# Kernel optimization log

Measured on AMD Instinct MI355X. Metric: run time of the kernel, lower is better.

## Reference

```python
import jax, jax.numpy as jnp
import numpy as np

EMBED = 2048
N_EXPERTS = 64
TOP_K = 8


def setup_inputs() -> dict:
    key = jax.random.key(0)
    k_x, k_w, k_b = jax.random.split(key, 3)
    inputs = jax.random.normal(k_x, (8, 4096, EMBED), dtype=jnp.float32)
    # nn.Linear(embed_size, num_experts): weight [E, D], bias [E]
    bound = 1.0 / np.sqrt(EMBED)
    W = jax.random.uniform(k_w, (N_EXPERTS, EMBED), dtype=jnp.float32, minval=-bound, maxval=bound)
    b = jax.random.uniform(k_b, (N_EXPERTS,), dtype=jnp.float32, minval=-bound, maxval=bound)
    return {"inputs": inputs, "W": W, "b": b}


def reference(inputs, W, b):
    # scores: [B, S, E]
    scores = jnp.einsum("bsd,ed->bse", inputs, W) + b
    topk_scores, indices = jax.lax.top_k(scores, TOP_K)  # [B,S,K]
    # scatter topk_scores into a zero mask (non-selected slots stay 0.0)
    onehot = jax.nn.one_hot(indices, N_EXPERTS, dtype=scores.dtype)  # [B,S,K,E]
    mask = jnp.einsum("bske,bsk->bse", onehot, topk_scores)
    router_output = jax.nn.softmax(mask, axis=-1)
    return (router_output, indices)
```

## Files before the change

kernel.cpp:

```cpp
#include <hip/hip_runtime.h>
#include <math.h>

#define N_TOKENS 32768
#define EMBED    2048
#define NEXP     64
#define TOPK     8
#define BM       64
#define BK       64
#define NCH      (EMBED / BK)
#define SCS      65
#define THRESH   1e-4f
#define WELEMS   (NEXP * EMBED)

typedef __attribute__((ext_vector_type(8)))  short short8;
typedef __attribute__((ext_vector_type(4)))  short short4v;
typedef __attribute__((ext_vector_type(16))) float f32x16;

__device__ __forceinline__ unsigned short bf16rne(float f) {
  unsigned int fb = __float_as_uint(f);
  return (unsigned short)((fb + 0x7FFFu + ((fb >> 16) & 1u)) >> 16);
}

__device__ __forceinline__ void cvt4(float4 f, short4v* h, short4v* l) {
  float fs[4] = {f.x, f.y, f.z, f.w};
  short4v hh, ll;
#pragma unroll
  for (int i = 0; i < 4; ++i) {
    unsigned short hr = bf16rne(fs[i]);
    hh[i] = (short)hr;
    float hf = __uint_as_float((unsigned int)hr << 16);
    ll[i] = (short)bf16rne(fs[i] - hf);
  }
  *h = hh; *l = ll;
}

__global__ void split_w(const float* __restrict__ W, short* __restrict__ wh,
                        short* __restrict__ wl) {
  const int T = blockIdx.x * 256 + threadIdx.x;
  const int n = T >> 8, kg8 = T & 255;
  const float4* W4 = (const float4*)W;
  float4 a = W4[n * 512 + kg8 * 2];
  float4 b = W4[n * 512 + kg8 * 2 + 1];
  short4v h0, l0, h1, l1;
  cvt4(a, &h0, &l0); cvt4(b, &h1, &l1);
  short* dh = &wh[(kg8 * 64 + n) * 8];
  short* dl = &wl[(kg8 * 64 + n) * 8];
  *(short4v*)dh = h0; *(short4v*)(dh + 4) = h1;
  *(short4v*)dl = l0; *(short4v*)(dl + 4) = l1;
}

__global__ __launch_bounds__(256, 4)
void router_kernel(const float* __restrict__ x, const short* __restrict__ wh,
                   const short* __restrict__ wl, const float* __restrict__ bias,
                   const float* __restrict__ Wf, float* __restrict__ out) {
  __shared__ float4 lx[2][1024];
  __shared__ double s_fix[NEXP];
  __shared__ int    s_list[BM];
  __shared__ int    s_cnt;
  float* sc = (float*)&lx[0][0];

  const int tid  = threadIdx.x;
  const int t0   = blockIdx.x * BM;
  const int lane = tid & 63;
  const int w    = tid >> 6;
  const int half = lane >> 5;
  const int r5   = lane & 31;
  const int tw   = (w & 1) * 32;
  const int ew   = (w >> 1) * 32;

  if (tid == 0) s_cnt = 0;

  const float4* x4g = (const float4*)x;
  const short8* Bh  = (const short8*)wh;
  const short8* Bl  = (const short8*)wl;
  const int boff = half * 64 + ew + r5;

  const int row16 = tid >> 4;
  const int s4    = tid & 15;
  const int c4sw  = s4 ^ row16;
  const int wbase = (tid & 192);

  f32x16 acc;
#pragma unroll
  for (int i = 0; i < 16; ++i) acc[i] = 0.f;

#pragma unroll
  for (int i = 0; i < 4; ++i) {
    const float4* gp = x4g + (size_t)(t0 + row16 + 16 * i) * (EMBED / 4) + c4sw;
    __builtin_amdgcn_global_load_lds((const void*)gp, (void*)&lx[0][i * 256 + wbase],
                                     16, 0, 0);
  }

  const int arow  = tw + r5;
  const int am    = arow & 15;
  const int abase = (arow >> 4) * 256 + am * 16;

  for (int ch = 0; ch < NCH; ++ch) {
    const int buf = ch & 1;
    __syncthreads();

    if (ch + 1 < NCH) {
#pragma unroll
      for (int i = 0; i < 4; ++i) {
        const float4* gp = x4g + (size_t)(t0 + row16 + 16 * i) * (EMBED / 4)
                               + (ch + 1) * 16 + c4sw;
        __builtin_amdgcn_global_load_lds((const void*)gp,
                                         (void*)&lx[buf ^ 1][i * 256 + wbase], 16, 0, 0);
      }
    }

    short8 bh[4], bl[4];
#pragma unroll
    for (int s = 0; s < 4; ++s) {
      const int bi = (ch * 4 + s) * 128 + boff;
      bh[s] = Bh[bi]; bl[s] = Bl[bi];
    }

#pragma unroll
    for (int s = 0; s < 4; ++s) {
      const int c0 = s * 4 + half * 2;
      float4 fa = lx[buf][abase + (c0 ^ am)];
      float4 fb = lx[buf][abase + ((c0 + 1) ^ am)];
      short4v h0, l0, h1, l1;
      cvt4(fa, &h0, &l0); cvt4(fb, &h1, &l1);
      short8 ah, al;
#pragma unroll
      for (int j = 0; j < 4; ++j) { ah[j] = h0[j]; ah[j + 4] = h1[j];
                                    al[j] = l0[j]; al[j + 4] = l1[j]; }
      acc = __builtin_amdgcn_mfma_f32_32x32x16_bf16(ah, bh[s], acc, 0, 0, 0);
      acc = __builtin_amdgcn_mfma_f32_32x32x16_bf16(ah, bl[s], acc, 0, 0, 0);
      acc = __builtin_amdgcn_mfma_f32_32x32x16_bf16(al, bh[s], acc, 0, 0, 0);
    }
  }

  __syncthreads();

#pragma unroll
  for (int reg = 0; reg < 16; ++reg) {
    const int row = (reg & 3) + 8 * (reg >> 2) + 4 * half;
    sc[(tw + row) * SCS + ew + r5] = acc[reg];
  }
  __syncthreads();

  float* rout = out;
  float* iout = out + (size_t)N_TOKENS * NEXP;
  const float bias_l = bias[lane];

  for (int tb = 0; tb < 4; ++tb) {
    const int tbase = w * 16 + tb * 4;
    float orig[4]; unsigned cur[4];
#pragma unroll
    for (int i = 0; i < 4; ++i) {
      orig[i] = sc[(tbase + i) * SCS + lane] + bias_l;
      unsigned b = __float_as_uint(orig[i]);
      unsigned u = b ^ (((unsigned)((int)b >> 31)) | 0x80000000u);
      cur[i] = (u & 0xFFFFFFC0u) | (63u - (unsigned)lane);
    }
    float m[4], Z[4], ming[4], prev[4], morig[4];
    int myidx[4]; bool sel[4];
#pragma unroll
    for (int i = 0; i < 4; ++i) { sel[i] = false; morig[i] = 0.f; myidx[i] = 0; ming[i] = 1e30f; }

#pragma unroll
    for (int r = 0; r < 9; ++r) {
      unsigned v[4];
#pragma unroll
      for (int i = 0; i < 4; ++i) v[i] = cur[i];
#pragma unroll
      for (int s2 = 1; s2 < 64; s2 <<= 1) {
#pragma unroll
        for (int i = 0; i < 4; ++i) {
          unsigned o = (unsigned)__shfl_xor((int)v[i], s2);
          v[i] = v[i] > o ? v[i] : o;
        }
      }
#pragma unroll
      for (int i = 0; i < 4; ++i) {
        unsigned vb = (v[i] & 0x80000000u) ? (v[i] ^ 0x80000000u) : ~v[i];
        float fv = __uint_as_float(vb);
        if (r == 0) { m[i] = fmaxf(fv, 0.f); Z[i] = 56.f * expf(-m[i]) + expf(fv - m[i]); }
        else {
          ming[i] = fminf(ming[i], prev[i] - fv);
          if (r < 8) Z[i] += expf(fv - m[i]);
        }
        prev[i] = fv;
        if (r < 8) {
          if (lane == r) myidx[i] = 63 - (int)(v[i] & 63u);
          if (cur[i] == v[i]) { sel[i] = true; morig[i] = orig[i]; cur[i] = 0u; }
        }
      }
    }
#pragma unroll
    for (int i = 0; i < 4; ++i) {
      const int t = tbase + i;
      if (ming[i] < THRESH) {
        if (lane == 0) { int p = atomicAdd(&s_cnt, 1); s_list[p] = t; }
      } else {
        const float p = expf(morig[i] - m[i]) / Z[i];
        rout[(size_t)(t0 + t) * NEXP + lane] = p;
        if (lane < TOPK) iout[(size_t)(t0 + t) * TOPK + lane] = (float)myidx[i];
      }
    }
  }

  __syncthreads();
  const int cnt = s_cnt;
  const float4* W4 = (const float4*)Wf;

  for (int i = 0; i < cnt; ++i) {
    const int t = s_list[i];
    const int e = tid >> 2, sub2 = tid & 3;
    const float4* xr = x4g + (size_t)(t0 + t) * (EMBED / 4) + sub2 * 128;
    const float4* wr = W4 + (size_t)e * (EMBED / 4) + sub2 * 128;
    double a0 = 0.0, a1 = 0.0;
#pragma unroll 4
    for (int m4 = 0; m4 < 128; m4 += 2) {
      float4 xv = xr[m4], wv = wr[m4];
      a0 = fma((double)xv.x, (double)wv.x, a0); a0 = fma((double)xv.y, (double)wv.y, a0);
      a0 = fma((double)xv.z, (double)wv.z, a0); a0 = fma((double)xv.w, (double)wv.w, a0);
      float4 xv2 = xr[m4 + 1], wv2 = wr[m4 + 1];
      a1 = fma((double)xv2.x, (double)wv2.x, a1); a1 = fma((double)xv2.y, (double)wv2.y, a1);
      a1 = fma((double)xv2.z, (double)wv2.z, a1); a1 = fma((double)xv2.w, (double)wv2.w, a1);
    }
    double a = a0 + a1;
    a += __shfl_xor(a, 1); a += __shfl_xor(a, 2);
    if (sub2 == 0) s_fix[e] = a + (double)bias[e];
    __syncthreads();

    if (tid < 64) {
      const double orig = s_fix[lane];
      double curd = orig, vals[8];
      int myidx = 0; double mym = 0.0;
#pragma unroll
      for (int r = 0; r < 8; ++r) {
        double v = curd; int id = lane;
#pragma unroll
        for (int s2 = 1; s2 < 64; s2 <<= 1) {
          const double ov = __shfl_xor(v, s2);
          const int    oi = __shfl_xor(id, s2);
          if (ov > v || (ov == v && oi < id)) { v = ov; id = oi; }
        }
        vals[r] = v;
        if (lane == r)  myidx = id;
        if (lane == id) { mym = orig; curd = -1e300; }
      }
      const double md = fmax(vals[0], 0.0);
      double Zd = 56.0 * exp(-md);
#pragma unroll
      for (int r = 0; r < 8; ++r) Zd += exp(vals[r] - md);
      const double p = exp(mym - md) / Zd;
      rout[(size_t)(t0 + t) * NEXP + lane] = (float)p;
      if (lane < TOPK) iout[(size_t)(t0 + t) * TOPK + lane] = (float)myidx;
    }
    __syncthreads();
  }
}

extern "C" void kernel_launch(void* const* d_in, const int* in_sizes, int n_in,
                              void* d_out, int out_size, void* d_ws, size_t ws_size,
                              hipStream_t stream) {
  const float* x = (const float*)d_in[0];
  const float* W = (const float*)d_in[1];
  const float* b = (const float*)d_in[2];
  short* wh = (short*)d_ws;
  short* wl = wh + WELEMS;
  split_w<<<64, 256, 0, stream>>>(W, wh, wl);
  router_kernel<<<N_TOKENS / BM, 256, 0, stream>>>(x, wh, wl, b, W, (float*)d_out);
}
```

Baseline: 558.0 us.

## Move near-tie fp64 fixup into a separate grid-wide kernel with global worklist

The router kernel no longer recomputes ambiguous tokens in fp64 inside each block. Instead it appends their global token ids to a global list through an atomic counter, and a new fixup kernel with a fixed grid walks that list. The fixup kernel stages x in shared memory and splits the 64 expert dot products across warps. This removes the per-block serial tail and the extra shared-memory and register pressure it put on the main GEMM kernel, and spreads the fixup work across many blocks. In exchange it adds a memset, a third launch and global atomics.

```diff
diff --git a/kernel.cpp b/kernel.cpp
--- a/kernel.cpp
+++ b/kernel.cpp
@@ -11,6 +11,7 @@
 #define SCS      65
 #define THRESH   1e-4f
 #define WELEMS   (NEXP * EMBED)
+#define FIXGRID  1024
 
 typedef __attribute__((ext_vector_type(8)))  short short8;
 typedef __attribute__((ext_vector_type(4)))  short short4v;
@@ -52,11 +53,9 @@
 __global__ __launch_bounds__(256, 4)
 void router_kernel(const float* __restrict__ x, const short* __restrict__ wh,
                    const short* __restrict__ wl, const float* __restrict__ bias,
-                   const float* __restrict__ Wf, float* __restrict__ out) {
+                   int* __restrict__ gcnt, int* __restrict__ glist,
+                   float* __restrict__ out) {
   __shared__ float4 lx[2][1024];
-  __shared__ double s_fix[NEXP];
-  __shared__ int    s_list[BM];
-  __shared__ int    s_cnt;
   float* sc = (float*)&lx[0][0];
 
   const int tid  = threadIdx.x;
@@ -68,8 +67,6 @@
   const int tw   = (w & 1) * 32;
   const int ew   = (w >> 1) * 32;
 
-  if (tid == 0) s_cnt = 0;
-
   const float4* x4g = (const float4*)x;
   const short8* Bh  = (const short8*)wh;
   const short8* Bl  = (const short8*)wl;
@@ -194,7 +191,7 @@
     for (int i = 0; i < 4; ++i) {
       const int t = tbase + i;
       if (ming[i] < THRESH) {
-        if (lane == 0) { int p = atomicAdd(&s_cnt, 1); s_list[p] = t; }
+        if (lane == 0) { int p = atomicAdd(gcnt, 1); glist[p] = t0 + t; }
       } else {
         const float p = expf(morig[i] - m[i]) / Z[i];
         rout[(size_t)(t0 + t) * NEXP + lane] = p;
@@ -202,33 +199,49 @@
       }
     }
   }
-
-  __syncthreads();
-  const int cnt = s_cnt;
-  const float4* W4 = (const float4*)Wf;
-
-  for (int i = 0; i < cnt; ++i) {
-    const int t = s_list[i];
-    const int e = tid >> 2, sub2 = tid & 3;
-    const float4* xr = x4g + (size_t)(t0 + t) * (EMBED / 4) + sub2 * 128;
-    const float4* wr = W4 + (size_t)e * (EMBED / 4) + sub2 * 128;
-    double a0 = 0.0, a1 = 0.0;
-#pragma unroll 4
-    for (int m4 = 0; m4 < 128; m4 += 2) {
-      float4 xv = xr[m4], wv = wr[m4];
-      a0 = fma((double)xv.x, (double)wv.x, a0); a0 = fma((double)xv.y, (double)wv.y, a0);
-      a0 = fma((double)xv.z, (double)wv.z, a0); a0 = fma((double)xv.w, (double)wv.w, a0);
-      float4 xv2 = xr[m4 + 1], wv2 = wr[m4 + 1];
-      a1 = fma((double)xv2.x, (double)wv2.x, a1); a1 = fma((double)xv2.y, (double)wv2.y, a1);
-      a1 = fma((double)xv2.z, (double)wv2.z, a1); a1 = fma((double)xv2.w, (double)wv2.w, a1);
-    }
-    double a = a0 + a1;
-    a += __shfl_xor(a, 1); a += __shfl_xor(a, 2);
-    if (sub2 == 0) s_fix[e] = a + (double)bias[e];
-    __syncthreads();
-
-    if (tid < 64) {
-      const double orig = s_fix[lane];
+}
+
+__global__ __launch_bounds__(256, 4)
+void fixup_kernel(const float* __restrict__ x, const float* __restrict__ Wf,
+                  const float* __restrict__ bias, const int* __restrict__ gcnt,
+                  const int* __restrict__ glist, float* __restrict__ out) {
+  __shared__ float4 xsh[512];
+  __shared__ double sco[NEXP];
+  const int tid  = threadIdx.x;
+  const int lane = tid & 63;
+  const int w    = tid >> 6;
+  float* rout = out;
+  float* iout = out + (size_t)N_TOKENS * NEXP;
+  const int cnt = *gcnt;
+
+  for (int j = blockIdx.x; j < cnt; j += FIXGRID) {
+    const int tok = glist[j];
+    const float4* xr = (const float4*)x + (size_t)tok * 512;
+    xsh[tid] = xr[tid];
+    xsh[tid + 256] = xr[tid + 256];
+    __syncthreads();
+
+    for (int i = 0; i < 16; ++i) {
+      const int e = w * 16 + i;
+      const float4* wr = (const float4*)Wf + (size_t)e * 512;
+      double a = 0.0;
+#pragma unroll
+      for (int q = 0; q < 8; ++q) {
+        float4 wv = wr[q * 64 + lane];
+        float4 xv = xsh[q * 64 + lane];
+        a = fma((double)xv.x, (double)wv.x, a);
+        a = fma((double)xv.y, (double)wv.y, a);
+        a = fma((double)xv.z, (double)wv.z, a);
+        a = fma((double)xv.w, (double)wv.w, a);
+      }
+#pragma unroll
+      for (int s2 = 1; s2 < 64; s2 <<= 1) a += __shfl_xor(a, s2);
+      if (lane == 0) sco[e] = a + (double)bias[e];
+    }
+    __syncthreads();
+
+    if (w == 0) {
+      const double orig = sco[lane];
       double curd = orig, vals[8];
       int myidx = 0; double mym = 0.0;
 #pragma unroll
@@ -249,8 +262,8 @@
 #pragma unroll
       for (int r = 0; r < 8; ++r) Zd += exp(vals[r] - md);
       const double p = exp(mym - md) / Zd;
-      rout[(size_t)(t0 + t) * NEXP + lane] = (float)p;
-      if (lane < TOPK) iout[(size_t)(t0 + t) * TOPK + lane] = (float)myidx;
+      rout[(size_t)tok * NEXP + lane] = (float)p;
+      if (lane < TOPK) iout[(size_t)tok * TOPK + lane] = (float)myidx;
     }
     __syncthreads();
   }
@@ -264,6 +277,12 @@
   const float* b = (const float*)d_in[2];
   short* wh = (short*)d_ws;
   short* wl = wh + WELEMS;
+  int* gcnt  = (int*)(wl + WELEMS);
+  int* glist = gcnt + 4;
+
+  hipMemsetAsync(gcnt, 0, 16, stream);
   split_w<<<64, 256, 0, stream>>>(W, wh, wl);
-  router_kernel<<<N_TOKENS / BM, 256, 0, stream>>>(x, wh, wl, b, W, (float*)d_out);
-}
+  router_kernel<<<N_TOKENS / BM, 256, 0, stream>>>(x, wh, wl, b, gcnt, glist,
+                                                   (float*)d_out);
+  fixup_kernel<<<FIXGRID, 256, 0, stream>>>(x, W, b, gcnt, glist, (float*)d_out);
+}
```

New measurement: 469.7 us. 1.19x faster.
